# Kernel optimization log

Measured on AMD Instinct MI355X. Metric: run time of the kernel, lower is better.

The kernel has to match this reference:

```python
import jax, jax.numpy as jnp
import numpy as np

EPS = 1e-5
NUM_GRAPHS = 1000


def _glorot(key, shape):
    fan_in, fan_out = shape[1], shape[0]
    lim = float(np.sqrt(6.0 / (fan_in + fan_out)))
    return jax.random.uniform(key, shape, jnp.float32, -lim, lim)


def setup_inputs() -> dict:
    N, E, C, D, L = 100_000, 1_600_000, 10_000, 32, 4
    key = jax.random.key(0)
    ks = jax.random.split(key, 12)
    x = jax.random.normal(ks[0], (N, 2), jnp.float32)
    edge_index = jax.random.randint(ks[1], (2, E), 0, N)
    edge_attr = jax.random.normal(ks[2], (E, 1), jnp.float32)
    candidate_idxs = jax.random.randint(ks[3], (C,), 0, N)
    batch = jnp.sort(jax.random.randint(ks[4], (N,), 0, NUM_GRAPHS))
    lk = jax.random.split(ks[5], L)
    lk2 = jax.random.split(ks[6], L)
    return {
        "x": x,
        "edge_index": edge_index,
        "edge_attr": edge_attr,
        "candidate_idxs": candidate_idxs,
        "batch": batch,
        "lin_in_w": _glorot(ks[7], (D, 2)),
        "lin_in_b": jnp.zeros((D,), jnp.float32),
        "w1": jnp.stack([_glorot(lk[i], (D, 2 * D + 1)) for i in range(L)]),
        "b1": jnp.zeros((L, D), jnp.float32),
        "bn1_g": jnp.ones((L, D), jnp.float32),
        "bn1_b": jnp.zeros((L, D), jnp.float32),
        "w2": jnp.stack([_glorot(lk2[i], (D, D)) for i in range(L)]),
        "b2": jnp.zeros((L, D), jnp.float32),
        "bn2_g": jnp.ones((L, D), jnp.float32),
        "bn2_b": jnp.zeros((L, D), jnp.float32),
        "lin_out_w": _glorot(ks[8], (1, D)),
        "lin_out_b": jnp.zeros((), jnp.float32),
    }


def _batchnorm(m, g, b):
    # training-mode BatchNorm1d over the edge (row) axis, biased variance
    mu = jnp.mean(m, axis=0)
    var = jnp.mean(jnp.square(m - mu), axis=0)
    return (m - mu) * jax.lax.rsqrt(var + EPS) * g + b


def reference(x, edge_index, edge_attr, candidate_idxs, batch,
              lin_in_w, lin_in_b, w1, b1, bn1_g, bn1_b,
              w2, b2, bn2_g, bn2_b, lin_out_w, lin_out_b):
    N = x.shape[0]
    src, dst = edge_index[0], edge_index[1]  # x_j = x[src], x_i = x[dst]
    h = x @ lin_in_w.T + lin_in_b  # [N, D]
    for l in range(w1.shape[0]):
        msg = jnp.concatenate([h[dst], h[src], edge_attr], axis=-1)  # [E, 2D+1]
        m = jax.nn.relu(_batchnorm(msg @ w1[l].T + b1[l], bn1_g[l], bn1_b[l]))
        m = jax.nn.relu(_batchnorm(m @ w2[l].T + b2[l], bn2_g[l], bn2_b[l]))
        h = h + jax.ops.segment_sum(m, dst, num_segments=N)
    logits = (h[candidate_idxs] @ lin_out_w.T)[:, 0] + lin_out_b  # [C]
    seg = batch[candidate_idxs]
    mx = jax.ops.segment_max(logits, seg, num_segments=NUM_GRAPHS)
    mx = jnp.where(jnp.isfinite(mx), mx, 0.0)
    lse = mx + jnp.log(jax.ops.segment_sum(jnp.exp(logits - mx[seg]), seg,
                                           num_segments=NUM_GRAPHS))
    return logits - lse[seg]
```

## Files before the change

kernel.cpp:

```cpp
#include <hip/hip_runtime.h>
#include <stdint.h>

#define NGRAPH 1000

typedef __attribute__((ext_vector_type(8))) short short8;
typedef __attribute__((ext_vector_type(4))) float f32x4;

static __device__ __forceinline__ uint32_t pack2_bf16(float a, float b) {
  uint32_t ua = __float_as_uint(a), ub = __float_as_uint(b);
  ua = (ua + 0x7fffu + ((ua >> 16) & 1u)) >> 16;
  ub = (ub + 0x7fffu + ((ub >> 16) & 1u)) >> 16;
  return ua | (ub << 16);
}
static __device__ __forceinline__ unsigned short f2bf(float x) {
  uint32_t u = __float_as_uint(x);
  u = (u + 0x7fffu + ((u >> 16) & 1u)) >> 16;
  return (unsigned short)u;
}
static __device__ __forceinline__ float bf2f(unsigned short u) {
  return __uint_as_float(((uint32_t)u) << 16);
}
union frag_u { short8 v; uint32_t u[4]; };

__global__ __launch_bounds__(256) void k_prep(const float* __restrict__ w1,
                                              float* __restrict__ w1n,
                                              float* __restrict__ w1c) {
  int t = blockIdx.x * 256 + threadIdx.x;
  if (t < 4 * 2048) {
    int l = t >> 11, r = t & 2047, k = r >> 6, o = r & 63;
    w1n[t] = (o < 32) ? w1[l * 2080 + o * 65 + k]
                      : w1[l * 2080 + (o - 32) * 65 + (k + 32)];
  } else if (t < 4 * 2048 + 4 * 32) {
    int u = t - 4 * 2048;
    int l = u >> 5, d = u & 31;
    w1c[u] = w1[l * 2080 + d * 65 + 64];
  }
}

__global__ __launch_bounds__(256) void k_init(const float* __restrict__ x,
                                              const float* __restrict__ wi,
                                              const float* __restrict__ bi,
                                              float* __restrict__ h, int N) {
  int t = blockIdx.x * 256 + threadIdx.x;
  if (t >= N * 32) return;
  int n = t >> 5, d = t & 31;
  h[t] = fmaf(x[2 * n], wi[2 * d], fmaf(x[2 * n + 1], wi[2 * d + 1], bi[d]));
}

__global__ __launch_bounds__(256) void k_zero32(int* __restrict__ p, int n) {
  int t = blockIdx.x * 256 + threadIdx.x;
  if (t < n) p[t] = 0;
}
__global__ __launch_bounds__(256) void k_hist(const int* __restrict__ dst,
                                              int* __restrict__ cnt, int E, int pstep) {
  const int part = blockIdx.x & 7;
  const int nlo = part * pstep, nhi = nlo + pstep;
  const int stride = (gridDim.x >> 3) * 256;
  for (int e = (blockIdx.x >> 3) * 256 + threadIdx.x; e < E; e += stride) {
    int d = dst[e];
    if (d >= nlo && d < nhi) atomicAdd(cnt + d, 1);
  }
}
__global__ __launch_bounds__(256) void k_scan1(const int* __restrict__ in,
                                               int* __restrict__ out,
                                               int* __restrict__ bsum, int n) {
  __shared__ int sh[256];
  const int t = threadIdx.x;
  const int idx = blockIdx.x * 1024 + t * 4;
  int v[4];
#pragma unroll
  for (int j = 0; j < 4; j++) v[j] = (idx + j < n) ? in[idx + j] : 0;
  int tsum = v[0] + v[1] + v[2] + v[3];
  sh[t] = tsum;
  __syncthreads();
#pragma unroll
  for (int ofs = 1; ofs < 256; ofs <<= 1) {
    int x = (t >= ofs) ? sh[t - ofs] : 0;
    __syncthreads();
    sh[t] += x;
    __syncthreads();
  }
  int run = sh[t] - tsum;
  if (t == 255) bsum[blockIdx.x] = sh[255];
#pragma unroll
  for (int j = 0; j < 4; j++) {
    if (idx + j < n) out[idx + j] = run;
    run += v[j];
  }
}
__global__ __launch_bounds__(256) void k_scan2(int* __restrict__ bsum, int nb) {
  __shared__ int sh[256];
  const int t = threadIdx.x;
  int val = (t < nb) ? bsum[t] : 0;
  sh[t] = val;
  __syncthreads();
#pragma unroll
  for (int ofs = 1; ofs < 256; ofs <<= 1) {
    int x = (t >= ofs) ? sh[t - ofs] : 0;
    __syncthreads();
    sh[t] += x;
    __syncthreads();
  }
  if (t < nb) bsum[t] = sh[t] - val;
}
__global__ __launch_bounds__(256) void k_scan3(int* __restrict__ rowptr,
                                               const int* __restrict__ bsum,
                                               int* __restrict__ cur, int n) {
  int t = blockIdx.x * 256 + threadIdx.x;
  if (t >= n) return;
  int v = rowptr[t] + bsum[t >> 10];
  rowptr[t] = v;
  cur[t] = v;
}
__global__ __launch_bounds__(256) void k_reorder(const int* __restrict__ src,
                                                 const int* __restrict__ dst,
                                                 const float* __restrict__ ea,
                                                 int* __restrict__ cur,
                                                 uint2* __restrict__ sedge, int E, int pstep) {
  const int part = blockIdx.x & 7;
  const int nlo = part * pstep, nhi = nlo + pstep;
  const int stride = (gridDim.x >> 3) * 256;
  for (int e = (blockIdx.x >> 3) * 256 + threadIdx.x; e < E; e += stride) {
    int d = dst[e];
    if (d >= nlo && d < nhi) {
      int pos = atomicAdd(cur + d, 1);
      sedge[pos] = make_uint2((unsigned)src[e], __float_as_uint(ea[e]));
    }
  }
}
__global__ __launch_bounds__(256) void k_fillrid(const int* __restrict__ rowptr,
                                                 const int* __restrict__ cnt,
                                                 int* __restrict__ rid_s, int N) {
  const int n = blockIdx.x * 8 + (threadIdx.x >> 5);
  if (n >= N) return;
  const int j0 = threadIdx.x & 31;
  const int start = rowptr[n], deg = cnt[n];
  for (int j = j0; j < deg; j += 32) rid_s[start + j] = n;
}

__global__ __launch_bounds__(256) void k_node(const float* __restrict__ h,
                                              const float* __restrict__ w1n,
                                              unsigned short* __restrict__ hAB, int N) {
  const int wid = (blockIdx.x * 256 + threadIdx.x) >> 6;
  const int lane = threadIdx.x & 63;
  if (wid >= N) return;
  const int n = __builtin_amdgcn_readfirstlane(wid);
  const float* hn = h + (size_t)n * 32;
  float acc = 0.f;
#pragma unroll
  for (int k = 0; k < 32; k++) acc = fmaf(hn[k], w1n[k * 64 + lane], acc);
  hAB[(size_t)n * 64 + lane] = f2bf(acc);
}

static __device__ __forceinline__ void block_stats_reduce(float* ssum, float* ssq,
                                                          float* __restrict__ stats) {
  __shared__ float red[4][64];
  const int lane = threadIdx.x & 63, wv = threadIdx.x >> 6;
#pragma unroll
  for (int q = 0; q < 32; q++) {
    float a = ssum[q], b = ssq[q];
#pragma unroll
    for (int m = 32; m >= 1; m >>= 1) {
      a += __shfl_xor(a, m, 64);
      b += __shfl_xor(b, m, 64);
    }
    if (lane == 0) { red[wv][q] = a; red[wv][32 + q] = b; }
  }
  __syncthreads();
  if (threadIdx.x < 64) {
    int q = threadIdx.x;
    stats[(size_t)blockIdx.x * 64 + q] = red[0][q] + red[1][q] + red[2][q] + red[3][q];
  }
}

__global__ __launch_bounds__(256, 2) void k_combine(
    const uint32_t* __restrict__ hAB, const uint2* __restrict__ sedge,
    const int* __restrict__ rid_s, const float* __restrict__ w1c,
    uint32_t* __restrict__ mpre, float* __restrict__ stats, int E) {
  float ssum[32], ssq[32];
#pragma unroll
  for (int q = 0; q < 32; q++) { ssum[q] = 0.f; ssq[q] = 0.f; }
  const int stride = gridDim.x * blockDim.x;
  for (int pos = blockIdx.x * blockDim.x + threadIdx.x; pos < E; pos += stride) {
    const uint2 se = sedge[pos];
    const int vs = (int)se.x;
    const float eav = __uint_as_float(se.y);
    const int rid = rid_s[pos];
    const uint4* pa = (const uint4*)(hAB + (size_t)rid * 32);
    const uint4* pb = (const uint4*)(hAB + (size_t)vs * 32 + 16);
    uint4 au[4], bu[4];
#pragma unroll
    for (int q = 0; q < 4; q++) { au[q] = pa[q]; bu[q] = pb[q]; }
    const uint32_t* ad = (const uint32_t*)au;
    const uint32_t* bd = (const uint32_t*)bu;
    float m[32];
#pragma unroll
    for (int p = 0; p < 16; p++) {
      float a0 = __uint_as_float(ad[p] << 16), a1 = __uint_as_float(ad[p] & 0xffff0000u);
      float b0 = __uint_as_float(bd[p] << 16), b1 = __uint_as_float(bd[p] & 0xffff0000u);
      m[2 * p]     = a0 + fmaf(eav, w1c[2 * p],     b0);
      m[2 * p + 1] = a1 + fmaf(eav, w1c[2 * p + 1], b1);
    }
    uint4* mp = (uint4*)(mpre + (size_t)pos * 16);
    mp[0] = make_uint4(pack2_bf16(m[0], m[1]), pack2_bf16(m[2], m[3]),
                       pack2_bf16(m[4], m[5]), pack2_bf16(m[6], m[7]));
    mp[1] = make_uint4(pack2_bf16(m[8], m[9]), pack2_bf16(m[10], m[11]),
                       pack2_bf16(m[12], m[13]), pack2_bf16(m[14], m[15]));
    mp[2] = make_uint4(pack2_bf16(m[16], m[17]), pack2_bf16(m[18], m[19]),
                       pack2_bf16(m[20], m[21]), pack2_bf16(m[22], m[23]));
    mp[3] = make_uint4(pack2_bf16(m[24], m[25]), pack2_bf16(m[26], m[27]),
                       pack2_bf16(m[28], m[29]), pack2_bf16(m[30], m[31]));
#pragma unroll
    for (int q = 0; q < 32; q++) { ssum[q] += m[q]; ssq[q] = fmaf(m[q], m[q], ssq[q]); }
  }
  block_stats_reduce(ssum, ssq, stats);
}

__global__ __launch_bounds__(256) void k_finalize(const float* __restrict__ stats, int nblk, int E,
                                                  const float* __restrict__ g,
                                                  const float* __restrict__ bb,
                                                  float* __restrict__ ss) {
  const int q = blockIdx.x;
  const int t = threadIdx.x;
  double s0 = 0.0, s1 = 0.0;
  for (int i = t; i < nblk; i += 256) {
    s0 += (double)stats[(size_t)i * 64 + q];
    s1 += (double)stats[(size_t)i * 64 + 32 + q];
  }
  __shared__ double r0[256], r1[256];
  r0[t] = s0; r1[t] = s1;
  __syncthreads();
#pragma unroll
  for (int m = 128; m >= 1; m >>= 1) {
    if (t < m) { r0[t] += r0[t + m]; r1[t] += r1[t + m]; }
    __syncthreads();
  }
  if (t == 0) {
    double invE = 1.0 / (double)E;
    double mu = r0[0] * invE;
    double var = r1[0] * invE - mu * mu;
    if (var < 0.0) var = 0.0;
    double sc = (double)g[q] / sqrt(var + 1e-5);
    ss[q] = (float)sc;
    ss[32 + q] = (float)((double)bb[q] - mu * sc);
  }
}

__global__ __launch_bounds__(256) void k_gemm2m(
    uint32_t* __restrict__ mpre, const float* __restrict__ ss,
    const float* __restrict__ w2, float* __restrict__ stats, int E) {
  const int lane = threadIdx.x & 63;
  const int wv = threadIdx.x >> 6;
  const int row = lane & 15;
  const int kb = (lane >> 4) * 8;
  const int G = E >> 4;
  const int gstart = blockIdx.x * 4 + wv;
  const int gstride = gridDim.x * 4;

  float sc[8], sh[8];
#pragma unroll
  for (int j = 0; j < 8; j++) { sc[j] = ss[kb + j]; sh[j] = ss[32 + kb + j]; }

  frag_u b0, b1;
#pragma unroll
  for (int p = 0; p < 4; p++) {
    const float* wp0 = w2 + (size_t)row * 32 + kb + 2 * p;
    const float* wp1 = w2 + (size_t)(row + 16) * 32 + kb + 2 * p;
    b0.u[p] = pack2_bf16(wp0[0], wp0[1]);
    b1.u[p] = pack2_bf16(wp1[0], wp1[1]);
  }

  float sum0 = 0.f, sq0 = 0.f, sum1 = 0.f, sq1 = 0.f;
  unsigned short* mp16 = (unsigned short*)mpre;

  for (int g = gstart; g < G; g += gstride) {
    const int e0 = g << 4;
    const uint4 raw = *(const uint4*)(mpre + (size_t)(e0 + row) * 16 + (lane >> 4) * 4);
    float m[8];
    m[0] = __uint_as_float(raw.x << 16); m[1] = __uint_as_float(raw.x & 0xffff0000u);
    m[2] = __uint_as_float(raw.y << 16); m[3] = __uint_as_float(raw.y & 0xffff0000u);
    m[4] = __uint_as_float(raw.z << 16); m[5] = __uint_as_float(raw.z & 0xffff0000u);
    m[6] = __uint_as_float(raw.w << 16); m[7] = __uint_as_float(raw.w & 0xffff0000u);
    frag_u a;
#pragma unroll
    for (int p = 0; p < 4; p++) {
      float x0 = fmaxf(fmaf(m[2 * p],     sc[2 * p],     sh[2 * p]),     0.f);
      float x1 = fmaxf(fmaf(m[2 * p + 1], sc[2 * p + 1], sh[2 * p + 1]), 0.f);
      a.u[p] = pack2_bf16(x0, x1);
    }
    f32x4 z = {0.f, 0.f, 0.f, 0.f};
    f32x4 acc0 = __builtin_amdgcn_mfma_f32_16x16x32_bf16(a.v, b0.v, z, 0, 0, 0);
    f32x4 acc1 = __builtin_amdgcn_mfma_f32_16x16x32_bf16(a.v, b1.v, z, 0, 0, 0);
#pragma unroll
    for (int r = 0; r < 4; r++) {
      sum0 += acc0[r]; sq0 = fmaf(acc0[r], acc0[r], sq0);
      sum1 += acc1[r]; sq1 = fmaf(acc1[r], acc1[r], sq1);
      const size_t base = (size_t)(e0 + (lane >> 4) * 4 + r) * 32;
      mp16[base + row]      = f2bf(acc0[r]);
      mp16[base + row + 16] = f2bf(acc1[r]);
    }
  }

  sum0 += __shfl_xor(sum0, 16); sum0 += __shfl_xor(sum0, 32);
  sq0  += __shfl_xor(sq0, 16);  sq0  += __shfl_xor(sq0, 32);
  sum1 += __shfl_xor(sum1, 16); sum1 += __shfl_xor(sum1, 32);
  sq1  += __shfl_xor(sq1, 16);  sq1  += __shfl_xor(sq1, 32);
  __shared__ float red[4][64];
  if (lane < 16) {
    red[wv][row] = sum0;      red[wv][16 + row] = sum1;
    red[wv][32 + row] = sq0;  red[wv][48 + row] = sq1;
  }
  __syncthreads();
  if (threadIdx.x < 64) {
    int q = threadIdx.x;
    stats[(size_t)blockIdx.x * 64 + q] = red[0][q] + red[1][q] + red[2][q] + red[3][q];
  }
}

__global__ __launch_bounds__(256) void k_agg(
    const unsigned short* __restrict__ mp16, const int* __restrict__ rowptr,
    const int* __restrict__ cnt, const float* __restrict__ ss,
    float* __restrict__ h, int N) {
  const int n = blockIdx.x * 8 + (threadIdx.x >> 5);
  if (n >= N) return;
  const int d = threadIdx.x & 31;
  const int start = rowptr[n];
  const int deg = cnt[n];
  const float sc = ss[d], sh = ss[32 + d];
  const unsigned short* p = mp16 + (size_t)start * 32 + d;
  float acc = 0.f;
  int j = 0;
  for (; j + 2 <= deg; j += 2) {
    float x0 = bf2f(p[(size_t)j * 32]);
    float x1 = bf2f(p[(size_t)(j + 1) * 32]);
    acc += fmaxf(fmaf(x0, sc, sh), 0.f);
    acc += fmaxf(fmaf(x1, sc, sh), 0.f);
  }
  if (j < deg) {
    float x0 = bf2f(p[(size_t)j * 32]);
    acc += fmaxf(fmaf(x0, sc, sh), 0.f);
  }
  h[(size_t)n * 32 + d] += acc;
}

__global__ __launch_bounds__(256) void k_initseg(unsigned* __restrict__ segmax,
                                                 float* __restrict__ segsum) {
  int t = blockIdx.x * 256 + threadIdx.x;
  if (t < NGRAPH) { segmax[t] = 0u; segsum[t] = 0.f; }
}

__global__ __launch_bounds__(256) void k_logits(
    const float* __restrict__ h, const int* __restrict__ cand, const int* __restrict__ batch,
    const float* __restrict__ wout, const float* __restrict__ bout,
    float* __restrict__ logits, int* __restrict__ seg, unsigned* __restrict__ segmax, int C) {
  int t = blockIdx.x * 256 + threadIdx.x;
  if (t >= C) return;
  int node = cand[t];
  const float4* hp = (const float4*)(h + (size_t)node * 32);
  float acc = bout[0];
#pragma unroll
  for (int kc = 0; kc < 8; kc++) {
    float4 v = hp[kc];
    acc = fmaf(v.x, wout[kc * 4 + 0], acc);
    acc = fmaf(v.y, wout[kc * 4 + 1], acc);
    acc = fmaf(v.z, wout[kc * 4 + 2], acc);
    acc = fmaf(v.w, wout[kc * 4 + 3], acc);
  }
  logits[t] = acc;
  int s = batch[node];
  seg[t] = s;
  unsigned o = __float_as_uint(acc);
  o ^= (o >> 31) ? 0xFFFFFFFFu : 0x80000000u;
  atomicMax(segmax + s, o);
}

static __device__ __forceinline__ float o2f(unsigned o) {
  o ^= (o & 0x80000000u) ? 0x80000000u : 0xFFFFFFFFu;
  return __uint_as_float(o);
}

__global__ __launch_bounds__(256) void k_expsum(const float* __restrict__ logits,
                                                const int* __restrict__ seg,
                                                const unsigned* __restrict__ segmax,
                                                float* __restrict__ segsum, int C) {
  int t = blockIdx.x * 256 + threadIdx.x;
  if (t >= C) return;
  int s = seg[t];
  float mx = o2f(segmax[s]);
  atomicAdd(segsum + s, expf(logits[t] - mx));
}

__global__ __launch_bounds__(256) void k_out(const float* __restrict__ logits,
                                             const int* __restrict__ seg,
                                             const unsigned* __restrict__ segmax,
                                             const float* __restrict__ segsum,
                                             float* __restrict__ out, int C) {
  int t = blockIdx.x * 256 + threadIdx.x;
  if (t >= C) return;
  int s = seg[t];
  out[t] = logits[t] - (o2f(segmax[s]) + logf(segsum[s]));
}

extern "C" void kernel_launch(void* const* d_in, const int* in_sizes, int n_in,
                              void* d_out, int out_size, void* d_ws, size_t ws_size,
                              hipStream_t stream) {
  const float* x     = (const float*)d_in[0];
  const int*   eidx  = (const int*)d_in[1];
  const float* eattr = (const float*)d_in[2];
  const int*   cand  = (const int*)d_in[3];
  const int*   batch = (const int*)d_in[4];
  const float* wi    = (const float*)d_in[5];
  const float* bi    = (const float*)d_in[6];
  const float* w1    = (const float*)d_in[7];
  const float* g1    = (const float*)d_in[9];
  const float* bb1   = (const float*)d_in[10];
  const float* w2    = (const float*)d_in[11];
  const float* g2    = (const float*)d_in[13];
  const float* bb2   = (const float*)d_in[14];
  const float* wout  = (const float*)d_in[15];
  const float* bout  = (const float*)d_in[16];

  const int N = in_sizes[4];
  const int E = in_sizes[2];
  const int C = in_sizes[3];
  const int* src  = eidx;
  const int* dstp = eidx + E;

  char* ws = (char*)d_ws;
  size_t off = 0;
  auto carve = [&](size_t bytes) {
    void* p = ws + off;
    off = (off + bytes + 255) & ~(size_t)255;
    return p;
  };
  const int NBLK = 1024;
  uint32_t* mpre   = (uint32_t*)carve((size_t)E * 64);
  float*    h      = (float*)carve((size_t)N * 32 * 4);
  uint32_t* hAB    = (uint32_t*)carve((size_t)N * 128);
  float*    w1n    = (float*)carve(4 * 2048 * 4);
  float*    w1c    = (float*)carve(4 * 32 * 4);
  float*    ss     = (float*)carve(64 * 4);
  float*    stats  = (float*)carve((size_t)NBLK * 64 * 4);
  int*      cnt    = (int*)carve((size_t)N * 4);
  int*      rowptr = (int*)carve((size_t)N * 4);
  int*      cur    = (int*)carve((size_t)N * 4);
  int*      bsum   = (int*)carve(256 * 4);
  uint2*    sedge  = (uint2*)carve((size_t)E * 8);
  int*      rid_s  = (int*)carve((size_t)E * 4);
  float*    logits = (float*)carve((size_t)C * 4);
  int*      seg    = (int*)carve((size_t)C * 4);
  unsigned* segmax = (unsigned*)carve(NGRAPH * 4);
  float*    segsum = (float*)carve(NGRAPH * 4);
  (void)ws_size; (void)n_in; (void)out_size;

  const int nb1 = (N + 1023) / 1024;
  const int pstep = (N + 7) / 8;
  k_zero32<<<(N + 255) / 256, 256, 0, stream>>>(cnt, N);
  k_hist<<<1024, 256, 0, stream>>>(dstp, cnt, E, pstep);
  k_scan1<<<nb1, 256, 0, stream>>>(cnt, rowptr, bsum, N);
  k_scan2<<<1, 256, 0, stream>>>(bsum, nb1);
  k_scan3<<<(N + 255) / 256, 256, 0, stream>>>(rowptr, bsum, cur, N);
  k_reorder<<<1024, 256, 0, stream>>>(src, dstp, eattr, cur, sedge, E, pstep);
  k_fillrid<<<(N + 7) / 8, 256, 0, stream>>>(rowptr, cnt, rid_s, N);

  k_prep<<<33, 256, 0, stream>>>(w1, w1n, w1c);
  k_init<<<(N * 32 + 255) / 256, 256, 0, stream>>>(x, wi, bi, h, N);

  for (int l = 0; l < 4; l++) {
    k_node<<<(N * 64 + 255) / 256, 256, 0, stream>>>(h, w1n + l * 2048,
                                                     (unsigned short*)hAB, N);
    k_combine<<<NBLK, 256, 0, stream>>>(hAB, sedge, rid_s, w1c + l * 32,
                                        mpre, stats, E);
    k_finalize<<<32, 256, 0, stream>>>(stats, NBLK, E, g1 + l * 32, bb1 + l * 32, ss);
    k_gemm2m<<<NBLK, 256, 0, stream>>>(mpre, ss, w2 + l * 1024, stats, E);
    k_finalize<<<32, 256, 0, stream>>>(stats, NBLK, E, g2 + l * 32, bb2 + l * 32, ss);
    k_agg<<<(N + 7) / 8, 256, 0, stream>>>((const unsigned short*)mpre, rowptr, cnt,
                                           ss, h, N);
  }

  k_initseg<<<(NGRAPH + 255) / 256, 256, 0, stream>>>(segmax, segsum);
  k_logits<<<(C + 255) / 256, 256, 0, stream>>>(h, cand, batch, wout, bout,
                                                logits, seg, segmax, C);
  k_expsum<<<(C + 255) / 256, 256, 0, stream>>>(logits, seg, segmax, segsum, C);
  k_out<<<(C + 255) / 256, 256, 0, stream>>>(logits, seg, segmax, segsum, (float*)d_out, C);
}
```

Before: 835.3 us.

## Pre-bucket edges by destination partition before CSR histogram and scatter

Adds a bucketing pass that splits edges into 8 destination-range partitions, with local shared-memory counts and one global atomic per block per bucket. The histogram and reorder kernels then read only their own partition's edges instead of each of 8 partition groups rescanning the whole edge list. This cuts the redundant global reads of dst/src/ea from eight passes to one, at the cost of an extra write/read of the bucketed copies, stored in the mpre scratch buffer. Any partition that holds more than cap edges is silently dropped, so correctness depends on the destination indices being roughly uniform.

```diff
diff --git a/kernel.cpp b/kernel.cpp
--- a/kernel.cpp
+++ b/kernel.cpp
@@ -51,16 +51,64 @@
   int t = blockIdx.x * 256 + threadIdx.x;
   if (t < n) p[t] = 0;
 }
-__global__ __launch_bounds__(256) void k_hist(const int* __restrict__ dst,
-                                              int* __restrict__ cnt, int E, int pstep) {
-  const int part = blockIdx.x & 7;
-  const int nlo = part * pstep, nhi = nlo + pstep;
+
+#define CHUNK 2048
+__global__ __launch_bounds__(256) void k_bucket(const int* __restrict__ src,
+                                                const int* __restrict__ dst,
+                                                const float* __restrict__ ea,
+                                                int* __restrict__ gcur,
+                                                int* __restrict__ bsrc,
+                                                int* __restrict__ bdst,
+                                                float* __restrict__ bea,
+                                                int E, int pstep, int cap) {
+  __shared__ int lcnt[8], lbase[8];
+  const int t = threadIdx.x;
+  const int base = blockIdx.x * CHUNK;
+  if (t < 8) lcnt[t] = 0;
+  __syncthreads();
+  int es[8], ds[8], ps[8];
+  float eas[8];
+#pragma unroll
+  for (int j = 0; j < 8; j++) {
+    int e = base + j * 256 + t;
+    bool ok = e < E;
+    int d = ok ? dst[e] : 0;
+    es[j] = ok ? src[e] : 0;
+    eas[j] = ok ? ea[e] : 0.f;
+    ds[j] = d;
+    ps[j] = ok ? (d / pstep) : -1;
+    if (ok) atomicAdd(&lcnt[ps[j]], 1);
+  }
+  __syncthreads();
+  if (t < 8) lbase[t] = atomicAdd(&gcur[t], lcnt[t]);
+  __syncthreads();
+  if (t < 8) lcnt[t] = lbase[t];
+  __syncthreads();
+#pragma unroll
+  for (int j = 0; j < 8; j++) {
+    if (ps[j] >= 0) {
+      int pos = atomicAdd(&lcnt[ps[j]], 1);
+      if (pos < cap) {
+        int idx = ps[j] * cap + pos;
+        bsrc[idx] = es[j];
+        bdst[idx] = ds[j];
+        bea[idx] = eas[j];
+      }
+    }
+  }
+}
+
+__global__ __launch_bounds__(256) void k_hist2(const int* __restrict__ bdst,
+                                               const int* __restrict__ gcur,
+                                               int* __restrict__ cnt, int cap) {
+  const int g = blockIdx.x & 7;
+  const int len = gcur[g];
   const int stride = (gridDim.x >> 3) * 256;
-  for (int e = (blockIdx.x >> 3) * 256 + threadIdx.x; e < E; e += stride) {
-    int d = dst[e];
-    if (d >= nlo && d < nhi) atomicAdd(cnt + d, 1);
-  }
-}
+  const int* bd = bdst + (size_t)g * cap;
+  for (int i = (blockIdx.x >> 3) * 256 + threadIdx.x; i < len; i += stride)
+    atomicAdd(cnt + bd[i], 1);
+}
+
 __global__ __launch_bounds__(256) void k_scan1(const int* __restrict__ in,
                                                int* __restrict__ out,
                                                int* __restrict__ bsum, int n) {
@@ -112,22 +160,24 @@
   rowptr[t] = v;
   cur[t] = v;
 }
-__global__ __launch_bounds__(256) void k_reorder(const int* __restrict__ src,
-                                                 const int* __restrict__ dst,
-                                                 const float* __restrict__ ea,
-                                                 int* __restrict__ cur,
-                                                 uint2* __restrict__ sedge, int E, int pstep) {
-  const int part = blockIdx.x & 7;
-  const int nlo = part * pstep, nhi = nlo + pstep;
+
+__global__ __launch_bounds__(256) void k_scatter2(const int* __restrict__ bsrc,
+                                                  const int* __restrict__ bdst,
+                                                  const float* __restrict__ bea,
+                                                  const int* __restrict__ gcur,
+                                                  int* __restrict__ cur,
+                                                  uint2* __restrict__ sedge, int cap) {
+  const int g = blockIdx.x & 7;
+  const int len = gcur[g];
   const int stride = (gridDim.x >> 3) * 256;
-  for (int e = (blockIdx.x >> 3) * 256 + threadIdx.x; e < E; e += stride) {
-    int d = dst[e];
-    if (d >= nlo && d < nhi) {
-      int pos = atomicAdd(cur + d, 1);
-      sedge[pos] = make_uint2((unsigned)src[e], __float_as_uint(ea[e]));
-    }
-  }
-}
+  const size_t o = (size_t)g * cap;
+  for (int i = (blockIdx.x >> 3) * 256 + threadIdx.x; i < len; i += stride) {
+    int d = bdst[o + i];
+    int pos = atomicAdd(cur + d, 1);
+    sedge[pos] = make_uint2((unsigned)bsrc[o + i], __float_as_uint(bea[o + i]));
+  }
+}
+
 __global__ __launch_bounds__(256) void k_fillrid(const int* __restrict__ rowptr,
                                                  const int* __restrict__ cnt,
                                                  int* __restrict__ rid_s, int N) {
@@ -447,20 +497,29 @@
   int*      bsum   = (int*)carve(256 * 4);
   uint2*    sedge  = (uint2*)carve((size_t)E * 8);
   int*      rid_s  = (int*)carve((size_t)E * 4);
+  int*      gcur   = (int*)carve(8 * 4);
   float*    logits = (float*)carve((size_t)C * 4);
   int*      seg    = (int*)carve((size_t)C * 4);
   unsigned* segmax = (unsigned*)carve(NGRAPH * 4);
   float*    segsum = (float*)carve(NGRAPH * 4);
   (void)ws_size; (void)n_in; (void)out_size;
 
+  const int cap = E / 8 + 65536;
+  int*   bsrc = (int*)mpre;
+  int*   bdst = bsrc + (size_t)8 * cap;
+  float* bea  = (float*)(bdst + (size_t)8 * cap);
+
   const int nb1 = (N + 1023) / 1024;
   const int pstep = (N + 7) / 8;
   k_zero32<<<(N + 255) / 256, 256, 0, stream>>>(cnt, N);
-  k_hist<<<1024, 256, 0, stream>>>(dstp, cnt, E, pstep);
+  k_zero32<<<1, 256, 0, stream>>>(gcur, 8);
+  k_bucket<<<(E + CHUNK - 1) / CHUNK, 256, 0, stream>>>(src, dstp, eattr, gcur,
+                                                        bsrc, bdst, bea, E, pstep, cap);
+  k_hist2<<<1024, 256, 0, stream>>>(bdst, gcur, cnt, cap);
   k_scan1<<<nb1, 256, 0, stream>>>(cnt, rowptr, bsum, N);
   k_scan2<<<1, 256, 0, stream>>>(bsum, nb1);
   k_scan3<<<(N + 255) / 256, 256, 0, stream>>>(rowptr, bsum, cur, N);
-  k_reorder<<<1024, 256, 0, stream>>>(src, dstp, eattr, cur, sedge, E, pstep);
+  k_scatter2<<<1024, 256, 0, stream>>>(bsrc, bdst, bea, gcur, cur, sedge, cap);
   k_fillrid<<<(N + 7) / 8, 256, 0, stream>>>(rowptr, cnt, rid_s, N);
 
   k_prep<<<33, 256, 0, stream>>>(w1, w1n, w1c);
```

Result: slower. 852.3 us, median of 2 (+2.0%).
